# Kernel tuning notes

Hardware: AMD Instinct MI355X
Metric: run time of the kernel (lower is better)

Reference implementation:

```python
import jax, jax.numpy as jnp
import numpy as np

B, N_PTS, N_IN = 1, 29696, 1024
E1, E2, E3, NZ = 512, 512, 2048, 32
D1, D2, D3 = 2048, 512, 512
K = 100
V_DOF = 1.0      # Student-t dof `v`
C_CONST = 1.0    # args.c
EPS = 1e-5


def setup_inputs() -> dict:
    key = jax.random.key(0)
    ks = jax.random.split(key, 24)

    def lin_w(k, din, dout):
        return (jax.random.normal(k, (din, dout), jnp.float32) / np.float32(np.sqrt(din)))

    return {
        "x": jax.random.normal(ks[0], (B, N_PTS, N_IN), jnp.float32),
        "t1_coordinate": jax.random.normal(ks[1], (B, N_PTS, 3), jnp.float32),
        "cluster_layer": jax.random.normal(ks[2], (B, K, NZ), jnp.float32),
        "We1": lin_w(ks[3], N_IN, E1), "be1": jnp.zeros((E1,), jnp.float32),
        "We2": lin_w(ks[4], E1, E2),   "be2": jnp.zeros((E2,), jnp.float32),
        "We3": lin_w(ks[5], E2, E3),   "be3": jnp.zeros((E3,), jnp.float32),
        "Wz":  lin_w(ks[6], E3, NZ),   "bz":  jnp.zeros((NZ,), jnp.float32),
        "Wd1": lin_w(ks[7], NZ, D1),   "bd1": jnp.zeros((D1,), jnp.float32),
        "Wd2": lin_w(ks[8], D1, D2),   "bd2": jnp.zeros((D2,), jnp.float32),
        "Wd3": lin_w(ks[9], D2, D3),   "bd3": jnp.zeros((D3,), jnp.float32),
        "Wxb": lin_w(ks[10], D3, N_IN), "bxb": jnp.zeros((N_IN,), jnp.float32),
    }


def _std(a, axis=-1, keepdims=True):
    # torch.std default is unbiased (ddof=1)
    return jnp.std(a, axis=axis, keepdims=keepdims, ddof=1)


def reference(x, t1_coordinate, cluster_layer,
              We1, be1, We2, be2, We3, be3, Wz, bz,
              Wd1, bd1, Wd2, bd2, Wd3, bd3, Wxb, bxb):
    relu = jax.nn.relu
    # --- AE encode / decode ---
    h = relu(x @ We1 + be1)
    h = relu(h @ We2 + be2)
    h = relu(h @ We3 + be3)
    z = h @ Wz + bz                                   # [B, N, NZ]
    d = relu(z @ Wd1 + bd1)
    d = relu(d @ Wd2 + bd2)
    d = relu(d @ Wd3 + bd3)
    x_bar = d @ Wxb + bxb                             # [B, N, N_IN]

    # --- positional modulation + per-point normalization ---
    t1 = t1_coordinate / 100.0
    cos_mult = jnp.prod(t1, axis=-1, keepdims=True) * 0.99 + 1.0   # [B, N, 1]
    zp = z * cos_mult                                 # with_pos=True
    zp = (zp - zp.mean(axis=-1, keepdims=True)) / _std(zp)

    # --- distance to cluster centers + (inverted) Student-t assignment ---
    # [B, N, K]
    dist = jnp.sum((zp[:, :, None, :] - cluster_layer[:, None, :, :]) ** 2, axis=-1)
    q = 1.0 / (EPS + dist / V_DOF)
    q = q ** (-(V_DOF + 1.0) / 2.0)
    q = q / jnp.sum(q, axis=-1, keepdims=True)
    predict = jnp.argmax(q, axis=-1)                  # [B, N] int

    # --- stat_target_distribution (batch_size == 1 path) ---
    index = q.shape[1]                                # N_PTS
    u = q.sum(axis=1, keepdims=True)                  # [B, 1, K]
    u = (u - u.mean(axis=-1, keepdims=True)) / _std(u)

    cnt = jnp.zeros((B, K), jnp.int32).at[jnp.arange(B)[:, None], predict].add(1)
    Ncnt = jnp.where(cnt > 0, cnt, 1).astype(q.dtype)  # torch.ones init for empty clusters

    temp_q = (1.0 - q) ** 2 * jnp.log(q) * index      # [B, N, K], negative
    # v_i = sum over flat(N*K) of sqrt(-N_i / temp_q) = sqrt(N_i) * S
    S = jnp.sum(jnp.sqrt(-1.0 / temp_q), axis=(1, 2))  # [B]
    v_vec = jnp.sqrt(Ncnt) * S[:, None]               # [B, K]
    v_vec = v_vec[:, None, :]                         # [B, 1, K]
    v_vec = (v_vec - v_vec.mean(axis=-1, keepdims=True)) / _std(v_vec)
    v_vec = jax.lax.stop_gradient(v_vec)              # computed under no_grad in torch

    # batch_size == 1: global min shift
    u = u - u.min() + 0.001
    v_vec = v_vec - v_vec.min() + 0.001

    f = u + v_vec + C_CONST                           # [B, 1, K]
    w1 = q ** 2 / f
    p0 = w1 / w1.sum(axis=-1, keepdims=True)
    # first step: self.p = p, then self.p = 0.1*p + 0.9*self.p.detach()
    p = 0.1 * p0 + 0.9 * jax.lax.stop_gradient(p0)

    # --- losses ---
    kl_loss = jnp.mean(p * (jnp.log(p) - jnp.log(q))) * 0.01
    re_loss = jnp.mean((x_bar - x) ** 2)
    D = jnp.sum((cluster_layer[:, :, None, :] - cluster_layer[:, None, :, :]) ** 2, axis=-1)
    mean_distance = D.sum() / (D.size - D.shape[0] * D.shape[1])
    u_loss = (1.0 / mean_distance) * 0.01
    loss = kl_loss + re_loss + u_loss
    return predict, loss
```

## Files before the change

### kernel.cpp

```cpp
#include <hip/hip_runtime.h>
#include <math.h>

#define M_PTS 29696
#define KCL 100
#define NZ_DIM 32

typedef _Float16 h8 __attribute__((ext_vector_type(8)));
typedef _Float16 h4 __attribute__((ext_vector_type(4)));
typedef float f4 __attribute__((ext_vector_type(4)));

__device__ __forceinline__ void load_lds16(const void* g, void* l) {
    __builtin_amdgcn_global_load_lds(
        (const __attribute__((address_space(1))) void*)g,
        (__attribute__((address_space(3))) void*)l, 16, 0, 0);
}

struct PrepW {
    const float* W[8];
    _Float16* Th[8];
    _Float16* Tl[8];
    int K[8];
    int N[8];
    int off[9];
};

__global__ __launch_bounds__(256)
void prep_weights(PrepW a)
{
    __shared__ float t[32][33];
    const int bid = blockIdx.x;
    int w = 0;
    #pragma unroll
    for (int i = 1; i < 8; ++i) w += (bid >= a.off[i]);
    const int local = bid - a.off[w];
    const int K = a.K[w], N = a.N[w];
    const int tx = N >> 5;
    const int sh = __builtin_ctz(tx);
    const int n0 = (local & (tx - 1)) * 32, k0 = (local >> sh) * 32;
    const float* W = a.W[w];
    _Float16* WTh = a.Th[w];
    _Float16* WTl = a.Tl[w];

    const int tid = threadIdx.x;
    {
        int r = tid / 8, c = (tid % 8) * 4;
        const float4 v = *(const float4*)(W + (size_t)(k0 + r) * N + n0 + c);
        t[r][c+0] = v.x; t[r][c+1] = v.y; t[r][c+2] = v.z; t[r][c+3] = v.w;
    }
    __syncthreads();
    {
        int r = tid / 8, c = (tid % 8) * 4;
        h4 hi, lo;
        #pragma unroll
        for (int u = 0; u < 4; ++u) {
            float f = t[c+u][r];
            _Float16 h = (_Float16)f;
            hi[u] = h; lo[u] = (_Float16)(f - (float)h);
        }
        *(h4*)(WTh + (size_t)(n0 + r) * K + k0 + c) = hi;
        *(h4*)(WTl + (size_t)(n0 + r) * K + k0 + c) = lo;
    }
}

__global__ __launch_bounds__(256)
void split_x_kernel(const float* __restrict__ x, _Float16* __restrict__ Xh,
                    _Float16* __restrict__ Xl, float* __restrict__ Zf,
                    float* __restrict__ U, int* __restrict__ CNT,
                    double* __restrict__ DBL)
{
    const int bid = blockIdx.x;
    if (bid < (M_PTS*NZ_DIM/4/256)) {
        const size_t zi = ((size_t)bid*256 + threadIdx.x)*4;
        *(float4*)(Zf + zi) = make_float4(0.0f, 0.0f, 0.0f, 0.0f);
    }
    if (bid == 0) {
        int t = threadIdx.x;
        if (t < KCL) { U[t] = 0.0f; CNT[t] = 0; }
        if (t < 8) DBL[t] = 0.0;
    }
    const size_t i = ((size_t)bid*256 + threadIdx.x)*4;
    const float4 v = *(const float4*)(x + i);
    float vv[4] = {v.x, v.y, v.z, v.w};
    h4 hi, lo;
    #pragma unroll
    for (int u = 0; u < 4; ++u) {
        _Float16 h = (_Float16)vv[u];
        hi[u] = h; lo[u] = (_Float16)(vv[u] - (float)h);
    }
    *(h4*)(Xh + i) = hi;
    *(h4*)(Xl + i) = lo;
}

template<int WM,int WN,int TM,int TN,bool RELU,int MODE,int TERMS>
__global__ __launch_bounds__(WM*WN*64)
void gemm_sp(const _Float16* __restrict__ Ahp, const _Float16* __restrict__ Alp,
             const _Float16* __restrict__ Bhp, const _Float16* __restrict__ Blp,
             const float* __restrict__ bias,
             _Float16* __restrict__ Ch, _Float16* __restrict__ Cl,
             float* __restrict__ Cf, const float* __restrict__ Xref,
             double* __restrict__ loss_acc,
             int M, int N, int K)
{
    constexpr int BM = WM*TM*16, BN = WN*TN*16, NW = WM*WN;
    constexpr int PL = (TERMS == 3) ? 2 : 1;
    constexpr int CA = BM/16, CB = BN/16;
    constexpr int STRIDE = PL*(BM+BN)*32;
    constexpr int NPW = ((MODE == 5) ? 1 : (CA/NW)*PL)
                      + ((CB >= NW) ? (CB/NW) : 1)*PL;
    constexpr int EXTRA = (MODE == 5) ? (2048 + 4096) : 0;
    __shared__ __align__(16) _Float16 smem[2*STRIDE + EXTRA];

    const int tid = threadIdx.x;
    const int wave = tid >> 6, lane = tid & 63;
    const int wm = wave / WN, wn = wave % WN;
    const int lrow = lane & 15, lq = lane >> 4;
    const int sw = (lrow >> 1) & 3;
    const int lr4 = lane >> 2, lc4 = lane & 3;
    const int bm0 = blockIdx.y * BM, bn0 = blockIdx.x * BN;

    f4 acc[TM][TN];
    #pragma unroll
    for (int i = 0; i < TM; ++i)
        #pragma unroll
        for (int j = 0; j < TN; ++j)
            acc[i][j] = (f4)0.0f;

    auto stage = [&](int s, int k0) {
        _Float16* base = smem + s*STRIDE;
        if constexpr (MODE == 5) {
            int r_in = lane >> 2;
            int gk = (lane & 3) ^ ((r_in >> 1) & 3);
            load_lds16(Alp + (size_t)(k0 + wn*16 + r_in)*32 + gk*8,
                       smem + 2*STRIDE + s*1024 + wn*512);
        } else {
            #pragma unroll
            for (int c = wave; c < CA; c += NW) {
                int r = c*16 + lr4;
                int g = lc4 ^ ((r >> 1) & 3);
                size_t goff = (size_t)(bm0 + r)*K + k0 + g*8;
                load_lds16(Ahp + goff, base + c*512);
                if (PL == 2) load_lds16(Alp + goff, base + BM*32 + c*512);
            }
        }
        if (CB >= NW) {
            #pragma unroll
            for (int c = wave; c < CB; c += NW) {
                int r = c*16 + lr4;
                int g = lc4 ^ ((r >> 1) & 3);
                size_t goff = (size_t)(bn0 + r)*K + k0 + g*8;
                load_lds16(Bhp + goff, base + PL*BM*32 + c*512);
                if (PL == 2) load_lds16(Blp + goff, base + PL*BM*32 + BN*32 + c*512);
            }
        } else {
            int c = wave % CB;
            int r = c*16 + lr4;
            int g = lc4 ^ ((r >> 1) & 3);
            size_t goff = (size_t)(bn0 + r)*K + k0 + g*8;
            load_lds16(Bhp + goff, base + PL*BM*32 + c*512);
            if (PL == 2) load_lds16(Blp + goff, base + PL*BM*32 + BN*32 + c*512);
        }
    };

    h8 zfr[(MODE == 5) ? TM : 1];
    auto computeA = [&](int ds, int s) {
        if constexpr (MODE == 5) {
            const _Float16* wslot = smem + 2*STRIDE + ds*1024 + wn*512;
            const float* bds = (const float*)(smem + 2*STRIDE + 2048);
            h8 wf = *(const h8*)(wslot + lrow*32 + ((lq ^ sw)*8));
            float bv = bds[s*32 + wn*16 + lrow];
            _Float16* areg = smem + ds*STRIDE;
            const int kc = wn*16 + lrow;
            #pragma unroll
            for (int i2 = 0; i2 < TM; ++i2) {
                f4 cc = __builtin_amdgcn_mfma_f32_16x16x32_f16(zfr[i2], wf, (f4)0.0f, 0, 0, 0);
                int cch = wm*TM + i2;
                #pragma unroll
                for (int r = 0; r < 4; ++r) {
                    float v = fmaxf(cc[r] + bv, 0.0f);
                    int r16 = lq*4 + r;
                    areg[cch*512 + r16*32 + (((kc >> 3) ^ ((r16 >> 1) & 3))*8) + (kc & 7)]
                        = (_Float16)v;
                }
            }
        }
    };

    if constexpr (MODE == 5) {
        #pragma unroll
        for (int c = wave; c < 8; c += NW)
            load_lds16(Xref + c*256 + lane*4, smem + 2*STRIDE + 2048 + c*512);
        #pragma unroll
        for (int i2 = 0; i2 < TM; ++i2)
            zfr[i2] = *(const h8*)(Ahp + (size_t)(bm0 + (wm*TM + i2)*16 + lrow)*32 + lq*8);
    }
    stage(0, 0);
    if constexpr (MODE == 5) {
        __builtin_amdgcn_s_waitcnt(0x0F70);
        __builtin_amdgcn_s_barrier();
        computeA(0, 0);
        asm volatile("s_waitcnt lgkmcnt(0)" ::: "memory");
        __builtin_amdgcn_s_barrier();
    }

    const int steps = K >> 5;
    for (int i = 0; i < steps; ++i) {
        const int sel = i & 1;
        if (i + 1 < steps) {
            stage(sel ^ 1, (i + 1) << 5);
            __builtin_amdgcn_s_waitcnt(0x0F70 | NPW);
        } else {
            __builtin_amdgcn_s_waitcnt(0x0F70);
        }
        __builtin_amdgcn_s_barrier();

        const _Float16* base = smem + sel*STRIDE;
        h8 ah[TM], al[TM], bh[TN], bl[TN];
        #pragma unroll
        for (int i2 = 0; i2 < TM; ++i2) {
            int row = (wm*TM + i2)*16 + lrow;
            int off = row*32 + ((lq ^ sw)*8);
            ah[i2] = *(const h8*)(base + off);
            if (PL == 2) al[i2] = *(const h8*)(base + BM*32 + off);
        }
        #pragma unroll
        for (int j = 0; j < TN; ++j) {
            int row = (wn*TN + j)*16 + lrow;
            int off = row*32 + ((lq ^ sw)*8);
            bh[j] = *(const h8*)(base + PL*BM*32 + off);
            if (PL == 2) bl[j] = *(const h8*)(base + PL*BM*32 + BN*32 + off);
        }
        if constexpr (MODE == 5) {
            if (i + 1 < steps) {
                __builtin_amdgcn_s_waitcnt(0x0F70 | (NPW - 1));
                computeA(sel ^ 1, i + 1);
            }
        }
        #pragma unroll
        for (int i2 = 0; i2 < TM; ++i2)
            #pragma unroll
            for (int j = 0; j < TN; ++j)
                acc[i2][j] = __builtin_amdgcn_mfma_f32_16x16x32_f16(ah[i2], bh[j], acc[i2][j], 0, 0, 0);
        if (TERMS == 3) {
            #pragma unroll
            for (int i2 = 0; i2 < TM; ++i2)
                #pragma unroll
                for (int j = 0; j < TN; ++j)
                    acc[i2][j] = __builtin_amdgcn_mfma_f32_16x16x32_f16(ah[i2], bl[j], acc[i2][j], 0, 0, 0);
            #pragma unroll
            for (int i2 = 0; i2 < TM; ++i2)
                #pragma unroll
                for (int j = 0; j < TN; ++j)
                    acc[i2][j] = __builtin_amdgcn_mfma_f32_16x16x32_f16(al[i2], bh[j], acc[i2][j], 0, 0, 0);
        }
        if constexpr (MODE == 5) {
            asm volatile("s_waitcnt lgkmcnt(0)" ::: "memory");
        }
        __builtin_amdgcn_s_barrier();
    }

    if constexpr (MODE == 4) {
        static_assert(WN*16 == 32, "MODE 4 needs N2=32 across WN waves");
        static_assert(BM*BN <= STRIDE, "MODE 4 tile planes must fit smem");
        constexpr int PLANE = BM*BN;
        constexpr int NC2 = BN/32;
        constexpr int MF2 = TM;
        const _Float16* Wh = (const _Float16*)Ch;
        const _Float16* Wl = (const _Float16*)Cl;
        _Float16* th = smem;
        _Float16* tl = smem + PLANE;

        const int n2 = wn*16 + lrow;
        h8 b2h[NC2], b2l[NC2];
        #pragma unroll
        for (int cc = 0; cc < NC2; ++cc) {
            size_t go = (size_t)n2*N + bn0 + cc*32 + lq*8;
            b2h[cc] = *(const h8*)(Wh + go);
            b2l[cc] = *(const h8*)(Wl + go);
        }

        #pragma unroll
        for (int j = 0; j < TN; ++j) {
            int col = (wn*TN + j)*16 + lrow;
            float bj = bias[bn0 + col];
            int c = col >> 5, kk = col & 31;
            #pragma unroll
            for (int i = 0; i < TM; ++i) {
                int m0 = (wm*TM + i)*16 + lq*4;
                #pragma unroll
                for (int r = 0; r < 4; ++r) {
                    float v = acc[i][j][r] + bj;
                    if (RELU) v = fmaxf(v, 0.0f);
                    int m = m0 + r;
                    int a = c*(BM*32) + m*32 + (((kk >> 3) ^ ((m >> 1) & 3))*8) + (kk & 7);
                    _Float16 hh = (_Float16)v;
                    th[a] = hh;
                    tl[a] = (_Float16)(v - (float)hh);
                }
            }
        }
        __syncthreads();

        f4 acc2[MF2];
        #pragma unroll
        for (int mf = 0; mf < MF2; ++mf) acc2[mf] = (f4)0.0f;
        #pragma unroll
        for (int mf = 0; mf < MF2; ++mf) {
            int mrow = (wm*TM + mf)*16 + lrow;
            #pragma unroll
            for (int cc = 0; cc < NC2; ++cc) {
                int off = cc*(BM*32) + mrow*32 + ((lq ^ sw)*8);
                h8 a2h = *(const h8*)(th + off);
                h8 a2l = *(const h8*)(tl + off);
                acc2[mf] = __builtin_amdgcn_mfma_f32_16x16x32_f16(a2h, b2h[cc], acc2[mf], 0, 0, 0);
                acc2[mf] = __builtin_amdgcn_mfma_f32_16x16x32_f16(a2h, b2l[cc], acc2[mf], 0, 0, 0);
                acc2[mf] = __builtin_amdgcn_mfma_f32_16x16x32_f16(a2l, b2h[cc], acc2[mf], 0, 0, 0);
            }
        }
        #pragma unroll
        for (int mf = 0; mf < MF2; ++mf) {
            int rb = bm0 + (wm*TM + mf)*16 + lq*4;
            #pragma unroll
            for (int r = 0; r < 4; ++r)
                atomicAdd(&Cf[(size_t)(rb + r)*32 + n2], acc2[mf][r]);
        }
        return;
    }

    float lsum = 0.0f;
    #pragma unroll
    for (int j = 0; j < TN; ++j) {
        int col = bn0 + (wn*TN + j)*16 + lrow;
        float bj = bias[col];
        #pragma unroll
        for (int i = 0; i < TM; ++i) {
            int rbase = bm0 + (wm*TM + i)*16 + lq*4;
            #pragma unroll
            for (int r = 0; r < 4; ++r) {
                float v = acc[i][j][r] + bj;
                if (RELU) v = fmaxf(v, 0.0f);
                size_t idx = (size_t)(rbase + r)*N + col;
                if (MODE == 2) {
                    float d = v - Xref[idx];
                    lsum = fmaf(d, d, lsum);
                } else if (MODE == 0) {
                    _Float16 hh = (_Float16)v;
                    __builtin_nontemporal_store(hh, &Ch[idx]);
                    __builtin_nontemporal_store((_Float16)(v - (float)hh), &Cl[idx]);
                } else if (MODE == 1) {
                    _Float16 hh = (_Float16)v;
                    __builtin_nontemporal_store(hh, &Ch[idx]);
                    __builtin_nontemporal_store(v, &Cf[idx]);
                } else {
                    __builtin_nontemporal_store((_Float16)v, &Ch[idx]);
                }
            }
        }
    }
    if (MODE == 2) {
        for (int off = 32; off > 0; off >>= 1) lsum += __shfl_down(lsum, off, 64);
        __syncthreads();
        float* sc = (float*)smem;
        if (lane == 0) sc[wave] = lsum;
        __syncthreads();
        if (tid == 0) {
            double t = 0.0;
            for (int w = 0; w < NW; ++w) t += (double)sc[w];
            atomicAdd(loss_acc, t);
        }
    }
}

__global__ __launch_bounds__(256)
void finish_z(float* __restrict__ zf, _Float16* __restrict__ zh, const float* __restrict__ bz)
{
    const size_t i = ((size_t)blockIdx.x*256 + threadIdx.x)*4;
    float4 v = *(const float4*)(zf + i);
    const int cb = (int)(i & 31);
    const float4 b = *(const float4*)(bz + cb);
    v.x += b.x; v.y += b.y; v.z += b.z; v.w += b.w;
    *(float4*)(zf + i) = v;
    h4 h;
    h[0] = (_Float16)v.x; h[1] = (_Float16)v.y; h[2] = (_Float16)v.z; h[3] = (_Float16)v.w;
    *(h4*)(zh + i) = h;
}

__global__ __launch_bounds__(256)
void cluster_pass(const float* __restrict__ z, const float* __restrict__ t1,
                  const float* __restrict__ clusters,
                  float* __restrict__ D, float* __restrict__ ROWSUM,
                  float* __restrict__ pred_out, float* __restrict__ u_acc,
                  int* __restrict__ cnt, double* __restrict__ S_acc)
{
    __shared__ float cl[KCL*33];
    __shared__ float u_s[KCL];
    __shared__ float swave[4];
    const int tid = threadIdx.x;
    const int lane = tid & 63;
    for (int i = tid; i < KCL*NZ_DIM; i += 256) cl[(i >> 5)*33 + (i & 31)] = clusters[i];
    if (tid < KCL) u_s[tid] = 0.0f;
    __syncthreads();

    const int p  = (blockIdx.x*256 + tid) >> 2;
    const int kg = tid & 3;

    float zr[NZ_DIM];
    const float a = t1[p*3+0]*0.01f, b = t1[p*3+1]*0.01f, c = t1[p*3+2]*0.01f;
    const float cm = a*b*c*0.99f + 1.0f;
    float mean = 0.0f;
    #pragma unroll
    for (int i = 0; i < NZ_DIM; ++i) { zr[i] = z[(size_t)p*NZ_DIM+i]*cm; mean += zr[i]; }
    mean *= (1.0f/NZ_DIM);
    float var = 0.0f;
    #pragma unroll
    for (int i = 0; i < NZ_DIM; ++i) { float d = zr[i]-mean; var += d*d; }
    const float istd = 1.0f / sqrtf(var * (1.0f/(NZ_DIM-1)));
    #pragma unroll
    for (int i = 0; i < NZ_DIM; ++i) zr[i] = (zr[i]-mean)*istd;

    float vals[25];
    float rowsum = 0.0f, best = -1.0f; int bk = 0;
    #pragma unroll
    for (int j = 0; j < 25; ++j) {
        const int k = kg + 4*j;
        float d = 0.0f;
        #pragma unroll
        for (int i = 0; i < NZ_DIM; ++i) { float t = zr[i]-cl[k*33+i]; d = fmaf(t,t,d); }
        float val = 1e-5f + d;
        vals[j] = val;
        rowsum += val;
        if (val > best) { best = val; bk = k; }
        D[(size_t)p*KCL + k] = val;
    }
    rowsum += __shfl_xor(rowsum, 1);
    rowsum += __shfl_xor(rowsum, 2);
    #pragma unroll
    for (int m = 1; m <= 2; m <<= 1) {
        float ov = __shfl_xor(best, m);
        int   ok = __shfl_xor(bk, m);
        if (ov > best || (ov == best && ok < bk)) { best = ov; bk = ok; }
    }
    if (kg == 0) {
        pred_out[p] = (float)bk;
        atomicAdd(&cnt[bk], 1);
        ROWSUM[p] = rowsum;
    }

    const float inv_rs = 1.0f/rowsum;
    float Sp = 0.0f;
    #pragma unroll
    for (int j = 0; j < 25; ++j) {
        float qv = vals[j]*inv_rs;
        float lq = logf(qv);
        float om = 1.0f - qv;
        Sp += sqrtf(-1.0f/(om*om*lq*(float)M_PTS));
        float qs = qv;
        qs += __shfl_xor(qs, 4);
        qs += __shfl_xor(qs, 8);
        qs += __shfl_xor(qs, 16);
        qs += __shfl_xor(qs, 32);
        if (lane < 4) atomicAdd(&u_s[lane + 4*j], qs);
    }
    for (int off = 32; off > 0; off >>= 1) Sp += __shfl_down(Sp, off, 64);
    if (lane == 0) swave[tid >> 6] = Sp;
    __syncthreads();
    if (tid < KCL) atomicAdd(&u_acc[tid], u_s[tid]);
    if (tid == 0) atomicAdd(S_acc, (double)(swave[0]+swave[1]+swave[2]+swave[3]));
}

__device__ __forceinline__ float blk_sum(float v, float* sh) {
    int tid = threadIdx.x;
    sh[tid] = v; __syncthreads();
    for (int s = 128; s > 0; s >>= 1) { if (tid < s) sh[tid] += sh[tid+s]; __syncthreads(); }
    float r = sh[0]; __syncthreads();
    return r;
}
__device__ __forceinline__ float blk_min(float v, float* sh) {
    int tid = threadIdx.x;
    sh[tid] = v; __syncthreads();
    for (int s = 128; s > 0; s >>= 1) { if (tid < s) sh[tid] = fminf(sh[tid], sh[tid+s]); __syncthreads(); }
    float r = sh[0]; __syncthreads();
    return r;
}

__global__ __launch_bounds__(256)
void finalize_kernel(const float* __restrict__ u_in, const int* __restrict__ cnt,
                     const double* __restrict__ dbl, const float* __restrict__ clusters,
                     float* __restrict__ f_out, double* __restrict__ dbl_out)
{
    __shared__ float sh[256];
    __shared__ double shd[256];
    const int tid = threadIdx.x;
    const bool act = (tid < KCL);
    const float S = (float)dbl[0];

    float uv = act ? u_in[tid] : 0.0f;
    float um = blk_sum(uv, sh) * (1.0f/KCL);
    float ud = act ? (uv - um) : 0.0f;
    float uvar = blk_sum(ud*ud, sh) * (1.0f/(KCL-1));
    float un = ud / sqrtf(uvar);
    float umin = blk_min(act ? un : 3.0e38f, sh);
    float ufin = un - umin + 0.001f;

    float vv = 0.0f;
    if (act) { int cc = cnt[tid]; if (cc < 1) cc = 1; vv = sqrtf((float)cc) * S; }
    float vm = blk_sum(vv, sh) * (1.0f/KCL);
    float vd = act ? (vv - vm) : 0.0f;
    float vvar = blk_sum(vd*vd, sh) * (1.0f/(KCL-1));
    float vn = vd / sqrtf(vvar);
    float vmin = blk_min(act ? vn : 3.0e38f, sh);
    float vfin = vn - vmin + 0.001f;

    if (act) f_out[tid] = ufin + vfin + 1.0f;

    double dp = 0.0;
    for (int pair = tid; pair < KCL*KCL; pair += 256) {
        int i = pair / KCL, j = pair % KCL;
        float d = 0.0f;
        #pragma unroll
        for (int t2 = 0; t2 < NZ_DIM; ++t2) {
            float x = clusters[i*NZ_DIM+t2] - clusters[j*NZ_DIM+t2];
            d = fmaf(x, x, d);
        }
        dp += (double)d;
    }
    shd[tid] = dp; __syncthreads();
    for (int s = 128; s > 0; s >>= 1) { if (tid < s) shd[tid] += shd[tid+s]; __syncthreads(); }
    if (tid == 0) {
        dbl_out[3] = 0.01 * (double)(KCL*KCL - KCL) / shd[0];
    }
}

__global__ __launch_bounds__(256)
void kl_pass(const float* __restrict__ D, const float* __restrict__ ROWSUM,
             const float* __restrict__ f, double* __restrict__ kl_acc)
{
    __shared__ float fs[KCL], lfs[KCL];
    __shared__ float swave[4];
    const int tid = threadIdx.x;
    const int lane = tid & 63;
    if (tid < KCL) { float fv = f[tid]; fs[tid] = fv; lfs[tid] = logf(fv); }
    __syncthreads();

    const int p  = (blockIdx.x*256 + tid) >> 2;
    const int kg = tid & 3;

    float vals[25];
    #pragma unroll
    for (int j = 0; j < 25; ++j) vals[j] = D[(size_t)p*KCL + kg + 4*j];

    float sv = 0.0f;
    #pragma unroll
    for (int j = 0; j < 25; ++j) { float v = vals[j]; sv += v*v/fs[kg + 4*j]; }
    sv += __shfl_xor(sv, 1);
    sv += __shfl_xor(sv, 2);

    const float rowsum = ROWSUM[p];
    const float lrs = logf(rowsum), lsv = logf(sv);
    const float inv_sv = 1.0f/sv;
    float klp = 0.0f;
    #pragma unroll
    for (int j = 0; j < 25; ++j) {
        const int k = kg + 4*j;
        float v = vals[j];
        float pv = v*v/fs[k]*inv_sv;
        klp += pv*(logf(v) - lfs[k] - lsv + lrs);
    }
    for (int off = 32; off > 0; off >>= 1) klp += __shfl_down(klp, off, 64);
    if (lane == 0) swave[tid >> 6] = klp;
    __syncthreads();
    if (tid == 0) atomicAdd(kl_acc, (double)(swave[0]+swave[1]+swave[2]+swave[3]));
}

__global__ void final_loss(const double* __restrict__ dbl, float* __restrict__ out)
{
    double kl = dbl[1] / (double)((size_t)M_PTS*KCL) * 0.01;
    double re = dbl[2] / (double)((size_t)M_PTS*1024);
    out[0] = (float)(kl + re + dbl[3]);
}

extern "C" void kernel_launch(void* const* d_in, const int* in_sizes, int n_in,
                              void* d_out, int out_size, void* d_ws, size_t ws_size,
                              hipStream_t stream)
{
    const float* x   = (const float*)d_in[0];
    const float* t1c = (const float*)d_in[1];
    const float* clu = (const float*)d_in[2];
    const float* We1 = (const float*)d_in[3];  const float* be1 = (const float*)d_in[4];
    const float* We2 = (const float*)d_in[5];  const float* be2 = (const float*)d_in[6];
    const float* We3 = (const float*)d_in[7];  const float* be3 = (const float*)d_in[8];
    const float* Wz  = (const float*)d_in[9];  const float* bz  = (const float*)d_in[10];
    const float* Wd1 = (const float*)d_in[11]; const float* bd1 = (const float*)d_in[12];
    const float* Wd2 = (const float*)d_in[13]; const float* bd2 = (const float*)d_in[14];
    const float* Wd3 = (const float*)d_in[15]; const float* bd3 = (const float*)d_in[16];
    const float* Wxb = (const float*)d_in[17]; const float* bxb = (const float*)d_in[18];
    float* out = (float*)d_out;

    const size_t M = M_PTS;
    _Float16* H = (_Float16*)d_ws;
    size_t o = 0;
    _Float16* BIGh = H + o; o += M*2048;
    _Float16* BIGl = H + o; o += M*2048;
    _Float16* S1h  = H + o; o += M*512;
    _Float16* S1l  = H + o; o += M*512;
    _Float16* S2h  = H + o; o += M*512;
    _Float16* S2l  = H + o; o += M*512;
    _Float16* Zh   = H + o; o += M*32;
    _Float16* Zl   = H + o; o += M*32;
    _Float16* We1h = H + o; o += 512*1024; _Float16* We1l = H + o; o += 512*1024;
    _Float16* We2h = H + o; o += 512*512;  _Float16* We2l = H + o; o += 512*512;
    _Float16* We3h = H + o; o += 2048*512; _Float16* We3l = H + o; o += 2048*512;
    _Float16* Wzh  = H + o; o += 32*2048;  _Float16* Wzl  = H + o; o += 32*2048;
    _Float16* Wd1h = H + o; o += 2048*32;  _Float16* Wd1l = H + o; o += 2048*32;
    _Float16* Wd2h = H + o; o += 512*2048; _Float16* Wd2l = H + o; o += 512*2048;
    _Float16* Wd3h = H + o; o += 512*512;  _Float16* Wd3l = H + o; o += 512*512;
    _Float16* Wxbh = H + o; o += 1024*512; _Float16* Wxbl = H + o; o += 1024*512;
    float* fpr = (float*)(H + o);
    float* Zf  = fpr;        fpr += M*32;
    float* U   = fpr;        fpr += 128;
    float* F   = fpr;        fpr += 128;
    int*   CNT = (int*)fpr;  fpr += 128;
    double* DBL = (double*)(((uintptr_t)fpr + 15) & ~(uintptr_t)15);

    _Float16* Xh = BIGh;
    _Float16* Xl = BIGh + M*1024;
    float* Dm  = (float*)S1l;
    float* RSm = (float*)S2l;

    split_x_kernel<<<(int)(M*1024/4/256), 256, 0, stream>>>(x, Xh, Xl, Zf, U, CNT, DBL);

    {
        PrepW pa;
        const float* Ws[8]  = {We1, We2, We3, Wz, Wd1, Wd2, Wd3, Wxb};
        _Float16* Ths[8]    = {We1h, We2h, We3h, Wzh, Wd1h, Wd2h, Wd3h, Wxbh};
        _Float16* Tls[8]    = {We1l, We2l, We3l, Wzl, Wd1l, Wd2l, Wd3l, Wxbl};
        const int Ks[8]     = {1024, 512, 512, 2048, 32, 2048, 512, 512};
        const int Ns[8]     = {512, 512, 2048, 32, 2048, 512, 512, 1024};
        int acc = 0;
        for (int i = 0; i < 8; ++i) {
            pa.W[i] = Ws[i]; pa.Th[i] = Ths[i]; pa.Tl[i] = Tls[i];
            pa.K[i] = Ks[i]; pa.N[i] = Ns[i];
            pa.off[i] = acc;
            acc += (Ns[i] >> 5) * (Ks[i] >> 5);
        }
        pa.off[8] = acc;
        prep_weights<<<acc, 256, 0, stream>>>(pa);
    }

    const int MB = M_PTS/128;
    gemm_sp<2,2,4,4,true ,0,3><<<dim3(4,  MB), 256, 0, stream>>>(Xh,  Xl,  We1h, We1l, be1, S1h, S1l, nullptr, nullptr, nullptr, M, 512,  1024);
    gemm_sp<2,2,4,4,true ,0,3><<<dim3(4,  MB), 256, 0, stream>>>(S1h, S1l, We2h, We2l, be2, S2h, S2l, nullptr, nullptr, nullptr, M, 512,  512);
    gemm_sp<2,2,4,4,true ,4,3><<<dim3(16, MB), 256, 0, stream>>>(S2h, S2l, We3h, We3l, be3, Wzh, Wzl, Zf, nullptr, nullptr, M, 2048, 512);
    finish_z<<<(int)(M*32/4/256), 256, 0, stream>>>(Zf, Zh, bz);
    gemm_sp<2,2,4,4,true ,5,1><<<dim3(4,  MB), 256, 0, stream>>>(Zh,  Wd1h, Wd2h, nullptr, bd2, S1h,  nullptr, nullptr, bd1, nullptr, M, 512,  2048);
    gemm_sp<2,2,4,4,true ,3,1><<<dim3(4,  MB), 256, 0, stream>>>(S1h, nullptr, Wd3h, nullptr, bd3, S2h,  nullptr, nullptr, nullptr, nullptr, M, 512,  512);
    gemm_sp<2,2,4,4,false,2,1><<<dim3(8,  MB), 256, 0, stream>>>(S2h, nullptr, Wxbh, nullptr, bxb, nullptr, nullptr, nullptr, x, DBL+2, M, 1024, 512);

    const int PB = (M_PTS*4)/256;
    cluster_pass<<<PB, 256, 0, stream>>>(Zf, t1c, clu, Dm, RSm, out, U, CNT, DBL + 0);
    finalize_kernel<<<1, 256, 0, stream>>>(U, CNT, DBL, clu, F, DBL);
    kl_pass<<<PB, 256, 0, stream>>>(Dm, RSm, F, DBL + 1);
    final_loss<<<1, 1, 0, stream>>>(DBL, out + M_PTS);
}
```

Measured before the change: 1.097 ms.

## Fuse fp16 split of x into first GEMM and fold z-bias into consumers

Removes the standalone kernel that split x into fp16 hi/lo halves; the first GEMM now loads fp32 x into registers, splits it, and writes both halves to LDS. The finish_z kernel is also removed: the z bias is added when the decoder GEMM loads z and inside cluster_pass. Buffer zero-initialisation moves into prep_weights. This saves a full write and re-read of x-sized intermediates, at the cost of synchronous register-staged A loads in the first GEMM, which may reduce load/compute overlap.

```diff
diff --git a/kernel.cpp b/kernel.cpp
--- a/kernel.cpp
+++ b/kernel.cpp
@@ -25,10 +25,22 @@
 };
 
 __global__ __launch_bounds__(256)
-void prep_weights(PrepW a)
+void prep_weights(PrepW a, float* __restrict__ Zf, float* __restrict__ U,
+                  int* __restrict__ CNT, double* __restrict__ DBL)
 {
     __shared__ float t[32][33];
     const int bid = blockIdx.x;
+    const int tid = threadIdx.x;
+
+    if (bid < (M_PTS*NZ_DIM/4/256)) {
+        const size_t zi = ((size_t)bid*256 + tid)*4;
+        *(float4*)(Zf + zi) = make_float4(0.0f, 0.0f, 0.0f, 0.0f);
+    }
+    if (bid == 0) {
+        if (tid < KCL) { U[tid] = 0.0f; CNT[tid] = 0; }
+        if (tid < 8) DBL[tid] = 0.0;
+    }
+
     int w = 0;
     #pragma unroll
     for (int i = 1; i < 8; ++i) w += (bid >= a.off[i]);
@@ -41,7 +53,6 @@
     _Float16* WTh = a.Th[w];
     _Float16* WTl = a.Tl[w];
 
-    const int tid = threadIdx.x;
     {
         int r = tid / 8, c = (tid % 8) * 4;
         const float4 v = *(const float4*)(W + (size_t)(k0 + r) * N + n0 + c);
@@ -62,36 +73,7 @@
     }
 }
 
-__global__ __launch_bounds__(256)
-void split_x_kernel(const float* __restrict__ x, _Float16* __restrict__ Xh,
-                    _Float16* __restrict__ Xl, float* __restrict__ Zf,
-                    float* __restrict__ U, int* __restrict__ CNT,
-                    double* __restrict__ DBL)
-{
-    const int bid = blockIdx.x;
-    if (bid < (M_PTS*NZ_DIM/4/256)) {
-        const size_t zi = ((size_t)bid*256 + threadIdx.x)*4;
-        *(float4*)(Zf + zi) = make_float4(0.0f, 0.0f, 0.0f, 0.0f);
-    }
-    if (bid == 0) {
-        int t = threadIdx.x;
-        if (t < KCL) { U[t] = 0.0f; CNT[t] = 0; }
-        if (t < 8) DBL[t] = 0.0;
-    }
-    const size_t i = ((size_t)bid*256 + threadIdx.x)*4;
-    const float4 v = *(const float4*)(x + i);
-    float vv[4] = {v.x, v.y, v.z, v.w};
-    h4 hi, lo;
-    #pragma unroll
-    for (int u = 0; u < 4; ++u) {
-        _Float16 h = (_Float16)vv[u];
-        hi[u] = h; lo[u] = (_Float16)(vv[u] - (float)h);
-    }
-    *(h4*)(Xh + i) = hi;
-    *(h4*)(Xl + i) = lo;
-}
-
-template<int WM,int WN,int TM,int TN,bool RELU,int MODE,int TERMS>
+template<int WM,int WN,int TM,int TN,bool RELU,int MODE,int TERMS,int ASRC=0>
 __global__ __launch_bounds__(WM*WN*64)
 void gemm_sp(const _Float16* __restrict__ Ahp, const _Float16* __restrict__ Alp,
              const _Float16* __restrict__ Bhp, const _Float16* __restrict__ Blp,
@@ -107,6 +89,9 @@
     constexpr int STRIDE = PL*(BM+BN)*32;
     constexpr int NPW = ((MODE == 5) ? 1 : (CA/NW)*PL)
                       + ((CB >= NW) ? (CB/NW) : 1)*PL;
+    constexpr int NPW_B = ((CB >= NW) ? (CB/NW) : 1)*PL;
+    static_assert(ASRC == 0 || (TERMS == 3 && (CA/NW) == 2 && MODE == 0),
+                  "ASRC=1 path sized for the L1 config");
     constexpr int EXTRA = (MODE == 5) ? (2048 + 4096) : 0;
     __shared__ __align__(16) _Float16 smem[2*STRIDE + EXTRA];
 
@@ -132,6 +117,7 @@
             int gk = (lane & 3) ^ ((r_in >> 1) & 3);
             load_lds16(Alp + (size_t)(k0 + wn*16 + r_in)*32 + gk*8,
                        smem + 2*STRIDE + s*1024 + wn*512);
+        } else if constexpr (ASRC == 1) {
         } else {
             #pragma unroll
             for (int c = wave; c < CA; c += NW) {
@@ -158,6 +144,39 @@
             size_t goff = (size_t)(bn0 + r)*K + k0 + g*8;
             load_lds16(Bhp + goff, base + PL*BM*32 + c*512);
             if (PL == 2) load_lds16(Blp + goff, base + PL*BM*32 + BN*32 + c*512);
+        }
+    };
+
+    auto stageA_load = [&](int k0, float4 (&ar)[4]) {
+        if constexpr (ASRC == 1) {
+            #pragma unroll
+            for (int u = 0; u < 2; ++u) {
+                int c = wave + u*NW;
+                int r = c*16 + lr4;
+                int g = lc4 ^ ((r >> 1) & 3);
+                const float* src = Xref + (size_t)(bm0 + r)*K + k0 + g*8;
+                ar[u*2+0] = *(const float4*)(src);
+                ar[u*2+1] = *(const float4*)(src + 4);
+            }
+        }
+    };
+    auto stageA_write = [&](int s, const float4 (&ar)[4]) {
+        if constexpr (ASRC == 1) {
+            _Float16* base = smem + s*STRIDE;
+            #pragma unroll
+            for (int u = 0; u < 2; ++u) {
+                int c = wave + u*NW;
+                float fv[8] = {ar[u*2].x, ar[u*2].y, ar[u*2].z, ar[u*2].w,
+                               ar[u*2+1].x, ar[u*2+1].y, ar[u*2+1].z, ar[u*2+1].w};
+                h8 hi, lo;
+                #pragma unroll
+                for (int q = 0; q < 8; ++q) {
+                    _Float16 h = (_Float16)fv[q];
+                    hi[q] = h; lo[q] = (_Float16)(fv[q] - (float)h);
+                }
+                *(h8*)(base + c*512 + lane*8) = hi;
+                *(h8*)(base + BM*32 + c*512 + lane*8) = lo;
+            }
         }
     };
 
@@ -185,15 +204,33 @@
         }
     };
 
+    float4 ar0[4];
+    if constexpr (ASRC == 1) stageA_load(0, ar0);
     if constexpr (MODE == 5) {
         #pragma unroll
         for (int c = wave; c < 8; c += NW)
             load_lds16(Xref + c*256 + lane*4, smem + 2*STRIDE + 2048 + c*512);
-        #pragma unroll
-        for (int i2 = 0; i2 < TM; ++i2)
-            zfr[i2] = *(const h8*)(Ahp + (size_t)(bm0 + (wm*TM + i2)*16 + lrow)*32 + lq*8);
+        const float* zf32 = (const float*)Ahp;
+        const float* bz32 = (const float*)Cl;
+        float4 b0 = *(const float4*)(bz32 + lq*8);
+        float4 b1 = *(const float4*)(bz32 + lq*8 + 4);
+        float bb[8] = {b0.x,b0.y,b0.z,b0.w,b1.x,b1.y,b1.z,b1.w};
+        #pragma unroll
+        for (int i2 = 0; i2 < TM; ++i2) {
+            const float* zsrc = zf32 + (size_t)(bm0 + (wm*TM + i2)*16 + lrow)*32 + lq*8;
+            float4 z0 = *(const float4*)(zsrc);
+            float4 z1 = *(const float4*)(zsrc + 4);
+            float zz[8] = {z0.x,z0.y,z0.z,z0.w,z1.x,z1.y,z1.z,z1.w};
+            #pragma unroll
+            for (int q = 0; q < 8; ++q) zfr[i2][q] = (_Float16)(zz[q] + bb[q]);
+        }
     }
     stage(0, 0);
+    if constexpr (ASRC == 1) {
+        __builtin_amdgcn_s_waitcnt(0x0F70 | NPW_B);
+        stageA_write(0, ar0);
+        asm volatile("s_waitcnt lgkmcnt(0)" ::: "memory");
+    }
     if constexpr (MODE == 5) {
         __builtin_amdgcn_s_waitcnt(0x0F70);
         __builtin_amdgcn_s_barrier();
@@ -205,7 +242,9 @@
     const int steps = K >> 5;
     for (int i = 0; i < steps; ++i) {
         const int sel = i & 1;
+        float4 arn[4];
         if (i + 1 < steps) {
+            if constexpr (ASRC == 1) stageA_load((i + 1) << 5, arn);
             stage(sel ^ 1, (i + 1) << 5);
             __builtin_amdgcn_s_waitcnt(0x0F70 | NPW);
         } else {
@@ -229,6 +268,12 @@
             bh[j] = *(const h8*)(base + PL*BM*32 + off);
             if (PL == 2) bl[j] = *(const h8*)(base + PL*BM*32 + BN*32 + off);
         }
+        if constexpr (ASRC == 1) {
+            if (i + 1 < steps) {
+                __builtin_amdgcn_s_waitcnt(0x0F70 | NPW_B);
+                stageA_write(sel ^ 1, arn);
+            }
+        }
         if constexpr (MODE == 5) {
             if (i + 1 < steps) {
                 __builtin_amdgcn_s_waitcnt(0x0F70 | (NPW - 1));
@@ -252,7 +297,7 @@
                 for (int j = 0; j < TN; ++j)
                     acc[i2][j] = __builtin_amdgcn_mfma_f32_16x16x32_f16(al[i2], bh[j], acc[i2][j], 0, 0, 0);
         }
-        if constexpr (MODE == 5) {
+        if constexpr (MODE == 5 || ASRC == 1) {
             asm volatile("s_waitcnt lgkmcnt(0)" ::: "memory");
         }
         __builtin_amdgcn_s_barrier();
@@ -371,21 +416,8 @@
 }
 
 __global__ __launch_bounds__(256)
-void finish_z(float* __restrict__ zf, _Float16* __restrict__ zh, const float* __restrict__ bz)
-{
-    const size_t i = ((size_t)blockIdx.x*256 + threadIdx.x)*4;
-    float4 v = *(const float4*)(zf + i);
-    const int cb = (int)(i & 31);
-    const float4 b = *(const float4*)(bz + cb);
-    v.x += b.x; v.y += b.y; v.z += b.z; v.w += b.w;
-    *(float4*)(zf + i) = v;
-    h4 h;
-    h[0] = (_Float16)v.x; h[1] = (_Float16)v.y; h[2] = (_Float16)v.z; h[3] = (_Float16)v.w;
-    *(h4*)(zh + i) = h;
-}
-
-__global__ __launch_bounds__(256)
-void cluster_pass(const float* __restrict__ z, const float* __restrict__ t1,
+void cluster_pass(const float* __restrict__ z, const float* __restrict__ bz,
+                  const float* __restrict__ t1,
                   const float* __restrict__ clusters,
                   float* __restrict__ D, float* __restrict__ ROWSUM,
                   float* __restrict__ pred_out, float* __restrict__ u_acc,
@@ -394,10 +426,12 @@
     __shared__ float cl[KCL*33];
     __shared__ float u_s[KCL];
     __shared__ float swave[4];
+    __shared__ float bzs[NZ_DIM];
     const int tid = threadIdx.x;
     const int lane = tid & 63;
     for (int i = tid; i < KCL*NZ_DIM; i += 256) cl[(i >> 5)*33 + (i & 31)] = clusters[i];
     if (tid < KCL) u_s[tid] = 0.0f;
+    if (tid < NZ_DIM) bzs[tid] = bz[tid];
     __syncthreads();
 
     const int p  = (blockIdx.x*256 + tid) >> 2;
@@ -408,7 +442,10 @@
     const float cm = a*b*c*0.99f + 1.0f;
     float mean = 0.0f;
     #pragma unroll
-    for (int i = 0; i < NZ_DIM; ++i) { zr[i] = z[(size_t)p*NZ_DIM+i]*cm; mean += zr[i]; }
+    for (int i = 0; i < NZ_DIM; ++i) {
+        zr[i] = (z[(size_t)p*NZ_DIM+i] + bzs[i])*cm;
+        mean += zr[i];
+    }
     mean *= (1.0f/NZ_DIM);
     float var = 0.0f;
     #pragma unroll
@@ -621,12 +658,8 @@
     int*   CNT = (int*)fpr;  fpr += 128;
     double* DBL = (double*)(((uintptr_t)fpr + 15) & ~(uintptr_t)15);
 
-    _Float16* Xh = BIGh;
-    _Float16* Xl = BIGh + M*1024;
     float* Dm  = (float*)S1l;
     float* RSm = (float*)S2l;
-
-    split_x_kernel<<<(int)(M*1024/4/256), 256, 0, stream>>>(x, Xh, Xl, Zf, U, CNT, DBL);
 
     {
         PrepW pa;
@@ -643,20 +676,19 @@
             acc += (Ns[i] >> 5) * (Ks[i] >> 5);
         }
         pa.off[8] = acc;
-        prep_weights<<<acc, 256, 0, stream>>>(pa);
+        prep_weights<<<acc, 256, 0, stream>>>(pa, Zf, U, CNT, DBL);
     }
 
     const int MB = M_PTS/128;
-    gemm_sp<2,2,4,4,true ,0,3><<<dim3(4,  MB), 256, 0, stream>>>(Xh,  Xl,  We1h, We1l, be1, S1h, S1l, nullptr, nullptr, nullptr, M, 512,  1024);
+    gemm_sp<2,2,4,4,true ,0,3,1><<<dim3(4,  MB), 256, 0, stream>>>(nullptr, nullptr, We1h, We1l, be1, S1h, S1l, nullptr, x, nullptr, M, 512,  1024);
     gemm_sp<2,2,4,4,true ,0,3><<<dim3(4,  MB), 256, 0, stream>>>(S1h, S1l, We2h, We2l, be2, S2h, S2l, nullptr, nullptr, nullptr, M, 512,  512);
     gemm_sp<2,2,4,4,true ,4,3><<<dim3(16, MB), 256, 0, stream>>>(S2h, S2l, We3h, We3l, be3, Wzh, Wzl, Zf, nullptr, nullptr, M, 2048, 512);
-    finish_z<<<(int)(M*32/4/256), 256, 0, stream>>>(Zf, Zh, bz);
-    gemm_sp<2,2,4,4,true ,5,1><<<dim3(4,  MB), 256, 0, stream>>>(Zh,  Wd1h, Wd2h, nullptr, bd2, S1h,  nullptr, nullptr, bd1, nullptr, M, 512,  2048);
+    gemm_sp<2,2,4,4,true ,5,1><<<dim3(4,  MB), 256, 0, stream>>>((const _Float16*)Zf, Wd1h, Wd2h, nullptr, bd2, S1h, (_Float16*)bz, nullptr, bd1, nullptr, M, 512,  2048);
     gemm_sp<2,2,4,4,true ,3,1><<<dim3(4,  MB), 256, 0, stream>>>(S1h, nullptr, Wd3h, nullptr, bd3, S2h,  nullptr, nullptr, nullptr, nullptr, M, 512,  512);
     gemm_sp<2,2,4,4,false,2,1><<<dim3(8,  MB), 256, 0, stream>>>(S2h, nullptr, Wxbh, nullptr, bxb, nullptr, nullptr, nullptr, x, DBL+2, M, 1024, 512);
 
     const int PB = (M_PTS*4)/256;
-    cluster_pass<<<PB, 256, 0, stream>>>(Zf, t1c, clu, Dm, RSm, out, U, CNT, DBL + 0);
+    cluster_pass<<<PB, 256, 0, stream>>>(Zf, bz, t1c, clu, Dm, RSm, out, U, CNT, DBL + 0);
     finalize_kernel<<<1, 256, 0, stream>>>(U, CNT, DBL, clu, F, DBL);
     kl_pass<<<PB, 256, 0, stream>>>(Dm, RSm, F, DBL + 1);
     final_loss<<<1, 1, 0, stream>>>(DBL, out + M_PTS);
```

Result: faster. 1.074 ms (-2.1%).
